# Performance work log

Measured on AMD Instinct MI355X. Metric: run time of the kernel, lower is better.

The kernel has to match this reference:

```python
import jax, jax.numpy as jnp
import numpy as np

U = 8  # LSTM units

def setup_inputs() -> dict:
    key = jax.random.key(0)
    ks = jax.random.split(key, 6)
    B, T, F = 4096, 512, 32
    x = jax.random.normal(ks[0], (B, T, F), dtype=jnp.float32)
    kernel = jax.random.normal(ks[1], (F, 4 * U), dtype=jnp.float32) * 0.1
    rec_kernel = jax.random.normal(ks[2], (U, 4 * U), dtype=jnp.float32) * 0.1
    bias = jnp.zeros((4 * U,), dtype=jnp.float32)
    w1 = jax.random.normal(ks[3], (U, 64), dtype=jnp.float32) * 0.1
    b1 = jnp.zeros((64,), dtype=jnp.float32)
    w2 = jax.random.normal(ks[4], (64, 4), dtype=jnp.float32) * 0.1
    b2 = jnp.zeros((4,), dtype=jnp.float32)
    return {"x": x, "kernel": kernel, "rec_kernel": rec_kernel, "bias": bias,
            "w1": w1, "b1": b1, "w2": w2, "b2": b2}

def _lstm_last_h(x, kernel, rec_kernel, bias):
    # Precompute input projections for all timesteps in one GEMM: [B,T,4U]
    xz = jnp.einsum('btf,fg->btg', x, kernel) + bias
    B = x.shape[0]
    h0 = jnp.zeros((B, U), dtype=x.dtype)
    c0 = jnp.zeros((B, U), dtype=x.dtype)

    def step(carry, xz_t):
        h, c = carry
        z = xz_t + h @ rec_kernel  # [B,4U]
        i = jax.nn.relu(z[:, 0 * U:1 * U])      # recurrent_activation='relu'
        f = jax.nn.relu(z[:, 1 * U:2 * U])
        g = jnp.tanh(z[:, 2 * U:3 * U])         # activation='tanh'
        o = jax.nn.relu(z[:, 3 * U:4 * U])
        c_new = f * c + i * g
        h_new = o * jnp.tanh(c_new)
        return (h_new, c_new), None

    (h_last, _), _ = jax.lax.scan(step, (h0, c0), jnp.swapaxes(xz, 0, 1))
    return h_last  # [B, U]

def reference(x, kernel, rec_kernel, bias, w1, b1, w2, b2):
    h = _lstm_last_h(x, kernel, rec_kernel, bias)
    h = jax.nn.relu(h @ w1 + b1)
    return jax.nn.sigmoid(h @ w2 + b2)  # [B, 4]
```

## Files before the change

### kernel.cpp

```cpp
#include <hip/hip_runtime.h>
#include <math.h>

#define BATCH   4096
#define TSTEPS  512
#define FDIM    32
#define UNITS   8
#define G4      32
#define CH      8
#define RPB     8

template<int PAT>
__device__ __forceinline__ float swzf(float v) {
    return __int_as_float(__builtin_amdgcn_ds_swizzle(__float_as_int(v), PAT));
}

__device__ __forceinline__ float fast_rcp(float x) { return __builtin_amdgcn_rcpf(x); }

__device__ __forceinline__ float fast_tanh(float x) {
    float e = __expf(2.0f * x);
    return 1.0f - 2.0f * fast_rcp(e + 1.0f);
}

__device__ __forceinline__ float sigmoidf_(float x) {
    return fast_rcp(1.0f + __expf(-x));
}

__global__ __launch_bounds__(256, 2)
void lstm_fused(const float* __restrict__ x,
                const float* __restrict__ kern,
                const float* __restrict__ rk,
                const float* __restrict__ bias,
                const float* __restrict__ w1,
                const float* __restrict__ b1,
                const float* __restrict__ w2,
                const float* __restrict__ b2,
                float* __restrict__ out)
{
    const int tid  = threadIdx.x;
    const int wv   = tid >> 6;
    const int half = (tid >> 5) & 1;
    const int j    = tid & 31;
    const int row  = blockIdx.x * RPB + wv * 2 + half;

    __shared__ __align__(16) float sx[2][4][2][CH * FDIM];

    float Kc[FDIM];
#pragma unroll
    for (int f = 0; f < FDIM; ++f) Kc[f] = kern[f * G4 + j];
    float Rc[UNITS];
#pragma unroll
    for (int u = 0; u < UNITS; ++u) Rc[u] = rk[u * G4 + j];
    const float bj  = bias[j];
    const bool  isg = ((j >> 3) == 2);

    const float* xrow = x + (size_t)row * (TSTEPS * FDIM);

    float h0=0.f,h1=0.f,h2=0.f,h3=0.f,h4=0.f,h5=0.f,h6=0.f,h7=0.f, c=0.f;

    float4 pa, pb;
    {
        const float4* p = (const float4*)xrow;
        float4 a = p[j], b = p[j + 32];
        float4* q = (float4*)&sx[0][wv][half][0];
        q[j] = a; q[j + 32] = b;
        const float4* p1 = (const float4*)(xrow + CH * FDIM);
        pa = p1[j]; pb = p1[j + 32];
    }

    int slot = 0;
    for (int tc = 0; tc < TSTEPS; tc += CH) {
        const float* xt0 = &sx[slot][wv][half][0];
#pragma unroll
        for (int k = 0; k < CH; ++k) {
            const float4* xv4 = (const float4*)(xt0 + k * FDIM);
            float z0 = bj, z1 = 0.f, z2 = 0.f, z3 = 0.f;
#pragma unroll
            for (int f0 = 0; f0 < 8; ++f0) {
                float4 xv = xv4[f0];
                z0 = fmaf(xv.x, Kc[4 * f0 + 0], z0);
                z1 = fmaf(xv.y, Kc[4 * f0 + 1], z1);
                z2 = fmaf(xv.z, Kc[4 * f0 + 2], z2);
                z3 = fmaf(xv.w, Kc[4 * f0 + 3], z3);
            }
            z0 = fmaf(h0, Rc[0], z0); z1 = fmaf(h1, Rc[1], z1);
            z2 = fmaf(h2, Rc[2], z2); z3 = fmaf(h3, Rc[3], z3);
            z0 = fmaf(h4, Rc[4], z0); z1 = fmaf(h5, Rc[5], z1);
            z2 = fmaf(h6, Rc[6], z2); z3 = fmaf(h7, Rc[7], z3);
            float z = (z0 + z1) + (z2 + z3);

            float a = isg ? fast_tanh(z) : fmaxf(z, 0.f);

            float ai = swzf<0x007>(a);
            float af = swzf<0x107>(a);
            float ag = swzf<0x207>(a);
            float ao = swzf<0x307>(a);

            c = fmaf(af, c, ai * ag);
            float hn = ao * fast_tanh(c);

            h0 = swzf<0x018>(hn); h1 = swzf<0x038>(hn);
            h2 = swzf<0x058>(hn); h3 = swzf<0x078>(hn);
            h4 = swzf<0x098>(hn); h5 = swzf<0x0B8>(hn);
            h6 = swzf<0x0D8>(hn); h7 = swzf<0x0F8>(hn);
        }
        if (tc + CH < TSTEPS) {
            float4* q = (float4*)&sx[slot ^ 1][wv][half][0];
            q[j] = pa; q[j + 32] = pb;
            if (tc + 2 * CH < TSTEPS) {
                const float4* p = (const float4*)(xrow + (tc + 2 * CH) * FDIM);
                pa = p[j]; pb = p[j + 32];
            }
            slot ^= 1;
        }
    }

    const float hh[8] = {h0, h1, h2, h3, h4, h5, h6, h7};
    float m0 = b1[j], m1 = b1[j + 32];
#pragma unroll
    for (int u = 0; u < 8; ++u) {
        m0 = fmaf(hh[u], w1[u * 64 + j],      m0);
        m1 = fmaf(hh[u], w1[u * 64 + 32 + j], m1);
    }
    m0 = fmaxf(m0, 0.f);
    m1 = fmaxf(m1, 0.f);

    float p0 = m0 * w2[j * 4 + 0] + m1 * w2[(j + 32) * 4 + 0];
    float p1 = m0 * w2[j * 4 + 1] + m1 * w2[(j + 32) * 4 + 1];
    float p2 = m0 * w2[j * 4 + 2] + m1 * w2[(j + 32) * 4 + 2];
    float p3 = m0 * w2[j * 4 + 3] + m1 * w2[(j + 32) * 4 + 3];

    p0 += swzf<0x041F>(p0); p1 += swzf<0x041F>(p1); p2 += swzf<0x041F>(p2); p3 += swzf<0x041F>(p3);
    p0 += swzf<0x081F>(p0); p1 += swzf<0x081F>(p1); p2 += swzf<0x081F>(p2); p3 += swzf<0x081F>(p3);
    p0 += swzf<0x101F>(p0); p1 += swzf<0x101F>(p1); p2 += swzf<0x101F>(p2); p3 += swzf<0x101F>(p3);
    p0 += swzf<0x201F>(p0); p1 += swzf<0x201F>(p1); p2 += swzf<0x201F>(p2); p3 += swzf<0x201F>(p3);
    p0 += swzf<0x401F>(p0); p1 += swzf<0x401F>(p1); p2 += swzf<0x401F>(p2); p3 += swzf<0x401F>(p3);

    if (j == 0) {
        float4 o;
        o.x = sigmoidf_(p0 + b2[0]);
        o.y = sigmoidf_(p1 + b2[1]);
        o.z = sigmoidf_(p2 + b2[2]);
        o.w = sigmoidf_(p3 + b2[3]);
        *(float4*)&out[row * 4] = o;
    }
}

extern "C" void kernel_launch(void* const* d_in, const int* in_sizes, int n_in,
                              void* d_out, int out_size, void* d_ws, size_t ws_size,
                              hipStream_t stream)
{
    const float* x    = (const float*)d_in[0];
    const float* kern = (const float*)d_in[1];
    const float* rk   = (const float*)d_in[2];
    const float* bias = (const float*)d_in[3];
    const float* w1   = (const float*)d_in[4];
    const float* b1   = (const float*)d_in[5];
    const float* w2   = (const float*)d_in[6];
    const float* b2   = (const float*)d_in[7];

    dim3 grid(BATCH / RPB);
    dim3 block(256);
    lstm_fused<<<grid, block, 0, stream>>>(x, kern, rk, bias, w1, b1, w2, b2, (float*)d_out);
}
```

Measured before the change: 435.1 us.

## Pack four LSTM rows per wavefront with two gates per lane and register prefetch

Each lane now computes two gate pre-activations, so one row needs only 16 lanes and a wavefront handles four rows. The grid shrinks to 256 blocks of 16 rows. The LDS double-buffer is replaced by a direct global-to-register triple-buffered prefetch of x timesteps. The aim is to halve the lanes spent per row and cut swizzle traffic on the recurrent critical path. In exchange, register use roughly doubles (two weight columns plus three buffered float4[8] sets), occupancy drops to one block per SIMD pair, and each lane issues its own global loads without LDS coalescing.

```diff
diff --git a/kernel.cpp b/kernel.cpp
--- a/kernel.cpp
+++ b/kernel.cpp
@@ -4,10 +4,6 @@
 #define BATCH   4096
 #define TSTEPS  512
 #define FDIM    32
-#define UNITS   8
-#define G4      32
-#define CH      8
-#define RPB     8
 
 template<int PAT>
 __device__ __forceinline__ float swzf(float v) {
@@ -25,7 +21,65 @@
     return fast_rcp(1.0f + __expf(-x));
 }
 
-__global__ __launch_bounds__(256, 2)
+struct LState {
+    float h0, h1, h2, h3, h4, h5, h6, h7, c;
+};
+
+__device__ __forceinline__ void ldx(float4 xv[8], const float4* __restrict__ p) {
+#pragma unroll
+    for (int i = 0; i < 8; ++i) xv[i] = p[i];
+}
+
+__device__ __forceinline__ void lstep(const float4 xv[8],
+                                      const float kc0[FDIM], const float kc1[FDIM],
+                                      const float rc0[8], const float rc1[8],
+                                      float ba, float bb, bool gp1, LState& s)
+{
+    float a0 = ba, a1 = 0.f, a2 = 0.f, a3 = 0.f;
+    float b0 = bb, b1 = 0.f, b2 = 0.f, b3 = 0.f;
+#pragma unroll
+    for (int f4 = 0; f4 < 8; ++f4) {
+        float4 xw = xv[f4];
+        a0 = fmaf(xw.x, kc0[4 * f4 + 0], a0);
+        a1 = fmaf(xw.y, kc0[4 * f4 + 1], a1);
+        a2 = fmaf(xw.z, kc0[4 * f4 + 2], a2);
+        a3 = fmaf(xw.w, kc0[4 * f4 + 3], a3);
+        b0 = fmaf(xw.x, kc1[4 * f4 + 0], b0);
+        b1 = fmaf(xw.y, kc1[4 * f4 + 1], b1);
+        b2 = fmaf(xw.z, kc1[4 * f4 + 2], b2);
+        b3 = fmaf(xw.w, kc1[4 * f4 + 3], b3);
+    }
+    a0 = fmaf(s.h0, rc0[0], a0); a1 = fmaf(s.h1, rc0[1], a1);
+    a2 = fmaf(s.h2, rc0[2], a2); a3 = fmaf(s.h3, rc0[3], a3);
+    a0 = fmaf(s.h4, rc0[4], a0); a1 = fmaf(s.h5, rc0[5], a1);
+    a2 = fmaf(s.h6, rc0[6], a2); a3 = fmaf(s.h7, rc0[7], a3);
+    b0 = fmaf(s.h0, rc1[0], b0); b1 = fmaf(s.h1, rc1[1], b1);
+    b2 = fmaf(s.h2, rc1[2], b2); b3 = fmaf(s.h3, rc1[3], b3);
+    b0 = fmaf(s.h4, rc1[4], b0); b1 = fmaf(s.h5, rc1[5], b1);
+    b2 = fmaf(s.h6, rc1[6], b2); b3 = fmaf(s.h7, rc1[7], b3);
+    float za = (a0 + a1) + (a2 + a3);
+    float zb = (b0 + b1) + (b2 + b3);
+
+    float va = gp1 ? fast_tanh(za) : fmaxf(za, 0.f);
+    float vb = fmaxf(zb, 0.f);
+
+    float pa = swzf<0x201F>(va);
+    float pb = swzf<0x201F>(vb);
+    float gi = gp1 ? pa : va;
+    float gf = gp1 ? pb : vb;
+    float gg = gp1 ? va : pa;
+    float go = gp1 ? vb : pb;
+
+    s.c = fmaf(gf, s.c, gi * gg);
+    float hn = go * fast_tanh(s.c);
+
+    s.h0 = swzf<0x010>(hn); s.h1 = swzf<0x030>(hn);
+    s.h2 = swzf<0x050>(hn); s.h3 = swzf<0x070>(hn);
+    s.h4 = swzf<0x090>(hn); s.h5 = swzf<0x0B0>(hn);
+    s.h6 = swzf<0x0D0>(hn); s.h7 = swzf<0x0F0>(hn);
+}
+
+__global__ __launch_bounds__(256, 1)
 void lstm_fused(const float* __restrict__ x,
                 const float* __restrict__ kern,
                 const float* __restrict__ rk,
@@ -36,112 +90,83 @@
                 const float* __restrict__ b2,
                 float* __restrict__ out)
 {
-    const int tid  = threadIdx.x;
-    const int wv   = tid >> 6;
-    const int half = (tid >> 5) & 1;
-    const int j    = tid & 31;
-    const int row  = blockIdx.x * RPB + wv * 2 + half;
+    const int tid = threadIdx.x;
+    const int wv  = tid >> 6;
+    const int l   = tid & 63;
+    const int u   = l & 7;
+    const int gp  = (l >> 3) & 1;
+    const int rl  = l >> 4;
+    const int row = blockIdx.x * 16 + wv * 4 + rl;
+    const bool gp1 = (gp != 0);
+    const int g0 = gp ? 16 + u : u;
+    const int g1 = gp ? 24 + u : 8 + u;
 
-    __shared__ __align__(16) float sx[2][4][2][CH * FDIM];
+    float kc0[FDIM], kc1[FDIM];
+#pragma unroll
+    for (int f = 0; f < FDIM; ++f) {
+        kc0[f] = kern[f * 32 + g0];
+        kc1[f] = kern[f * 32 + g1];
+    }
+    float rc0[8], rc1[8];
+#pragma unroll
+    for (int i = 0; i < 8; ++i) {
+        rc0[i] = rk[i * 32 + g0];
+        rc1[i] = rk[i * 32 + g1];
+    }
+    const float ba = bias[g0], bb = bias[g1];
 
-    float Kc[FDIM];
+    const float4* xr = (const float4*)(x + (size_t)row * (TSTEPS * FDIM));
+
+    LState s = {0.f, 0.f, 0.f, 0.f, 0.f, 0.f, 0.f, 0.f, 0.f};
+
+    float4 X0[8], X1[8], X2[8];
+    ldx(X0, xr + 0 * 8);
+    ldx(X1, xr + 1 * 8);
+    ldx(X2, xr + 2 * 8);
+
+    for (int tb = 0; tb < 510; tb += 3) {
+        lstep(X0, kc0, kc1, rc0, rc1, ba, bb, gp1, s);
+        ldx(X0, xr + (size_t)min(tb + 3, TSTEPS - 1) * 8);
+        lstep(X1, kc0, kc1, rc0, rc1, ba, bb, gp1, s);
+        ldx(X1, xr + (size_t)min(tb + 4, TSTEPS - 1) * 8);
+        lstep(X2, kc0, kc1, rc0, rc1, ba, bb, gp1, s);
+        ldx(X2, xr + (size_t)min(tb + 5, TSTEPS - 1) * 8);
+    }
+    lstep(X0, kc0, kc1, rc0, rc1, ba, bb, gp1, s);
+    lstep(X1, kc0, kc1, rc0, rc1, ba, bb, gp1, s);
+
+    const int q = l & 15;
+    const float hh[8] = {s.h0, s.h1, s.h2, s.h3, s.h4, s.h5, s.h6, s.h7};
+    float m[4];
 #pragma unroll
-    for (int f = 0; f < FDIM; ++f) Kc[f] = kern[f * G4 + j];
-    float Rc[UNITS];
+    for (int k = 0; k < 4; ++k) {
+        const int cc = q * 4 + k;
+        float mm = b1[cc];
 #pragma unroll
-    for (int u = 0; u < UNITS; ++u) Rc[u] = rk[u * G4 + j];
-    const float bj  = bias[j];
-    const bool  isg = ((j >> 3) == 2);
+        for (int hu = 0; hu < 8; ++hu) mm = fmaf(hh[hu], w1[hu * 64 + cc], mm);
+        m[k] = fmaxf(mm, 0.f);
+    }
+    float s0 = 0.f, s1 = 0.f, s2 = 0.f, s3 = 0.f;
+#pragma unroll
+    for (int k = 0; k < 4; ++k) {
+        const int cc = q * 4 + k;
+        s0 = fmaf(m[k], w2[cc * 4 + 0], s0);
+        s1 = fmaf(m[k], w2[cc * 4 + 1], s1);
+        s2 = fmaf(m[k], w2[cc * 4 + 2], s2);
+        s3 = fmaf(m[k], w2[cc * 4 + 3], s3);
+    }
+    s0 += swzf<0x041F>(s0); s1 += swzf<0x041F>(s1); s2 += swzf<0x041F>(s2); s3 += swzf<0x041F>(s3);
+    s0 += swzf<0x081F>(s0); s1 += swzf<0x081F>(s1); s2 += swzf<0x081F>(s2); s3 += swzf<0x081F>(s3);
+    s0 += swzf<0x101F>(s0); s1 += swzf<0x101F>(s1); s2 += swzf<0x101F>(s2); s3 += swzf<0x101F>(s3);
+    s0 += swzf<0x201F>(s0); s1 += swzf<0x201F>(s1); s2 += swzf<0x201F>(s2); s3 += swzf<0x201F>(s3);
 
-    const float* xrow = x + (size_t)row * (TSTEPS * FDIM);
-
-    float h0=0.f,h1=0.f,h2=0.f,h3=0.f,h4=0.f,h5=0.f,h6=0.f,h7=0.f, c=0.f;
-
-    float4 pa, pb;
-    {
-        const float4* p = (const float4*)xrow;
-        float4 a = p[j], b = p[j + 32];
-        float4* q = (float4*)&sx[0][wv][half][0];
-        q[j] = a; q[j + 32] = b;
-        const float4* p1 = (const float4*)(xrow + CH * FDIM);
-        pa = p1[j]; pb = p1[j + 32];
-    }
-
-    int slot = 0;
-    for (int tc = 0; tc < TSTEPS; tc += CH) {
-        const float* xt0 = &sx[slot][wv][half][0];
-#pragma unroll
-        for (int k = 0; k < CH; ++k) {
-            const float4* xv4 = (const float4*)(xt0 + k * FDIM);
-            float z0 = bj, z1 = 0.f, z2 = 0.f, z3 = 0.f;
-#pragma unroll
-            for (int f0 = 0; f0 < 8; ++f0) {
-                float4 xv = xv4[f0];
-                z0 = fmaf(xv.x, Kc[4 * f0 + 0], z0);
-                z1 = fmaf(xv.y, Kc[4 * f0 + 1], z1);
-                z2 = fmaf(xv.z, Kc[4 * f0 + 2], z2);
-                z3 = fmaf(xv.w, Kc[4 * f0 + 3], z3);
-            }
-            z0 = fmaf(h0, Rc[0], z0); z1 = fmaf(h1, Rc[1], z1);
-            z2 = fmaf(h2, Rc[2], z2); z3 = fmaf(h3, Rc[3], z3);
-            z0 = fmaf(h4, Rc[4], z0); z1 = fmaf(h5, Rc[5], z1);
-            z2 = fmaf(h6, Rc[6], z2); z3 = fmaf(h7, Rc[7], z3);
-            float z = (z0 + z1) + (z2 + z3);
-
-            float a = isg ? fast_tanh(z) : fmaxf(z, 0.f);
-
-            float ai = swzf<0x007>(a);
-            float af = swzf<0x107>(a);
-            float ag = swzf<0x207>(a);
-            float ao = swzf<0x307>(a);
-
-            c = fmaf(af, c, ai * ag);
-            float hn = ao * fast_tanh(c);
-
-            h0 = swzf<0x018>(hn); h1 = swzf<0x038>(hn);
-            h2 = swzf<0x058>(hn); h3 = swzf<0x078>(hn);
-            h4 = swzf<0x098>(hn); h5 = swzf<0x0B8>(hn);
-            h6 = swzf<0x0D8>(hn); h7 = swzf<0x0F8>(hn);
-        }
-        if (tc + CH < TSTEPS) {
-            float4* q = (float4*)&sx[slot ^ 1][wv][half][0];
-            q[j] = pa; q[j + 32] = pb;
-            if (tc + 2 * CH < TSTEPS) {
-                const float4* p = (const float4*)(xrow + (tc + 2 * CH) * FDIM);
-                pa = p[j]; pb = p[j + 32];
-            }
-            slot ^= 1;
-        }
-    }
-
-    const float hh[8] = {h0, h1, h2, h3, h4, h5, h6, h7};
-    float m0 = b1[j], m1 = b1[j + 32];
-#pragma unroll
-    for (int u = 0; u < 8; ++u) {
-        m0 = fmaf(hh[u], w1[u * 64 + j],      m0);
-        m1 = fmaf(hh[u], w1[u * 64 + 32 + j], m1);
-    }
-    m0 = fmaxf(m0, 0.f);
-    m1 = fmaxf(m1, 0.f);
-
-    float p0 = m0 * w2[j * 4 + 0] + m1 * w2[(j + 32) * 4 + 0];
-    float p1 = m0 * w2[j * 4 + 1] + m1 * w2[(j + 32) * 4 + 1];
-    float p2 = m0 * w2[j * 4 + 2] + m1 * w2[(j + 32) * 4 + 2];
-    float p3 = m0 * w2[j * 4 + 3] + m1 * w2[(j + 32) * 4 + 3];
-
-    p0 += swzf<0x041F>(p0); p1 += swzf<0x041F>(p1); p2 += swzf<0x041F>(p2); p3 += swzf<0x041F>(p3);
-    p0 += swzf<0x081F>(p0); p1 += swzf<0x081F>(p1); p2 += swzf<0x081F>(p2); p3 += swzf<0x081F>(p3);
-    p0 += swzf<0x101F>(p0); p1 += swzf<0x101F>(p1); p2 += swzf<0x101F>(p2); p3 += swzf<0x101F>(p3);
-    p0 += swzf<0x201F>(p0); p1 += swzf<0x201F>(p1); p2 += swzf<0x201F>(p2); p3 += swzf<0x201F>(p3);
-    p0 += swzf<0x401F>(p0); p1 += swzf<0x401F>(p1); p2 += swzf<0x401F>(p2); p3 += swzf<0x401F>(p3);
-
-    if (j == 0) {
+    if (q == 0) {
         float4 o;
-        o.x = sigmoidf_(p0 + b2[0]);
-        o.y = sigmoidf_(p1 + b2[1]);
-        o.z = sigmoidf_(p2 + b2[2]);
-        o.w = sigmoidf_(p3 + b2[3]);
-        *(float4*)&out[row * 4] = o;
+        o.x = sigmoidf_(s0 + b2[0]);
+        o.y = sigmoidf_(s1 + b2[1]);
+        o.z = sigmoidf_(s2 + b2[2]);
+        o.w = sigmoidf_(s3 + b2[3]);
+        *(float4*)&out[(size_t)row * 4] = o;
     }
 }
 
@@ -158,7 +183,7 @@
     const float* w2   = (const float*)d_in[6];
     const float* b2   = (const float*)d_in[7];
 
-    dim3 grid(BATCH / RPB);
+    dim3 grid(BATCH / 16);
     dim3 block(256);
     lstm_fused<<<grid, block, 0, stream>>>(x, kern, rk, bias, w1, b1, w2, b2, (float*)d_out);
 }
```

Result: slower. 505.2 us (+16.1%).
